# Optimization experiments

Measured on AMD Instinct MI355X. Metric: run time of the kernel, lower is better.

The kernel has to match this reference:

```python
import jax, jax.numpy as jnp
import numpy as np

TOP_K = 2


def setup_inputs() -> dict:
    key = jax.random.key(0)
    k1, k2, k3, k4, k5 = jax.random.split(key, 5)
    B, S, H, F, E = 4, 2048, 1024, 4096, 8
    scale = 1.0 / np.sqrt(H)
    return {
        "hidden_states": jax.random.normal(k1, (B, S, H), dtype=jnp.float32),
        "gate_w": jax.random.normal(k2, (E, H), dtype=jnp.float32) * scale,
        "w1": jax.random.normal(k3, (E, F, H), dtype=jnp.float32) * scale,
        "w3": jax.random.normal(k4, (E, F, H), dtype=jnp.float32) * scale,
        "w2": jax.random.normal(k5, (E, H, F), dtype=jnp.float32) * (1.0 / np.sqrt(F)),
    }


def reference(hidden_states, gate_w, w1, w3, w2):
    B, S, H = hidden_states.shape
    E = gate_w.shape[0]
    x = hidden_states.reshape(-1, H)                    # [T, H], T = B*S

    router_logits = x @ gate_w.T                        # [T, E]
    probs = jax.nn.softmax(router_logits.astype(jnp.float32), axis=-1)
    top_w, top_i = jax.lax.top_k(probs, TOP_K)          # [T, k]
    top_w = top_w / jnp.sum(top_w, axis=-1, keepdims=True)
    top_w = top_w.astype(x.dtype)

    # combine weight of each expert for each token: [E, T]
    one_hot = jax.nn.one_hot(top_i, E, dtype=x.dtype)   # [T, k, E]
    comb = jnp.einsum("tke,tk->et", one_hot, top_w)

    # loop over experts via scan; tokens not routed to expert e have comb==0,
    # which matches the gather/FFN/scatter-combine of the original exactly.
    def body(acc, wts):
        w1e, w3e, w2e, ce = wts
        h = jax.nn.silu(x @ w1e.T) * (x @ w3e.T)        # [T, F]
        return acc + (h @ w2e.T) * ce[:, None], None

    out0 = jnp.zeros_like(x)
    out, _ = jax.lax.scan(body, out0, (w1, w3, w2, comb))
    return out.reshape(B, S, H), router_logits
```

## Files before the change

kernel.cpp:

```cpp
#include <hip/hip_runtime.h>
#include <hip/hip_bf16.h>

#define T_TOK 8192
#define HDIM  1024
#define FDIM  4096
#define NEXP  8
#define CVT_BLKS 2048

typedef __attribute__((ext_vector_type(8))) short short8;
typedef __attribute__((ext_vector_type(4))) float f32x4;
typedef unsigned short u16;
typedef unsigned int   u32;

#define XB_OFF    0ull
#define W1B_OFF   (XB_OFF   + 16777216ull)
#define W3B_OFF   (W1B_OFF  + 67108864ull)
#define W2B_OFF   (W3B_OFF  + 67108864ull)
#define HBUF_OFF  (W2B_OFF  + 67108864ull)
#define CNT_OFF   (HBUF_OFF + 134217728ull)
#define HOFF_OFF  (CNT_OFF  + 64ull)
#define TLIST_OFF (HOFF_OFF + 64ull)
#define WLIST_OFF (TLIST_OFF + 262144ull)
#define WS_NEED   (WLIST_OFF + 262144ull)

__device__ __forceinline__ u16 f2bf(float f) {
  u32 u = __float_as_uint(f);
  return (u16)((u + 0x7fffu + ((u >> 16) & 1u)) >> 16);
}

__device__ __forceinline__ void gl_lds16(const void* g, void* l) {
  __builtin_amdgcn_global_load_lds(
      (const __attribute__((address_space(1))) void*)g,
      (__attribute__((address_space(3))) void*)l, 16, 0, 0);
}

__global__ __launch_bounds__(256) void prep_kernel(
    const float* __restrict__ x, const float* __restrict__ gw,
    const float* __restrict__ s0, const float* __restrict__ s1,
    u16* __restrict__ d0, u16* __restrict__ d1,
    float* __restrict__ logits, u16* __restrict__ xb,
    int* __restrict__ counts, int* __restrict__ tlist, float* __restrict__ wlist) {
  if (blockIdx.x < 8192) {
    const int n8 = NEXP * FDIM * HDIM / 8;
    const int total = 2 * n8;
    const int stride = 8192 * 256;
    for (int i = blockIdx.x * 256 + threadIdx.x; i < total; i += stride) {
      int seg = i >> 22;
      int j = i & (n8 - 1);
      const float* s = seg == 0 ? s0 : s1;
      u16* d = seg == 0 ? d0 : d1;
      float4 v0 = ((const float4*)s)[j * 2];
      float4 v1 = ((const float4*)s)[j * 2 + 1];
      uint4 o;
      o.x = (u32)f2bf(v0.x) | ((u32)f2bf(v0.y) << 16);
      o.y = (u32)f2bf(v0.z) | ((u32)f2bf(v0.w) << 16);
      o.z = (u32)f2bf(v1.x) | ((u32)f2bf(v1.y) << 16);
      o.w = (u32)f2bf(v1.z) | ((u32)f2bf(v1.w) << 16);
      ((uint4*)d)[j] = o;
    }
    return;
  }
  const int wid = threadIdx.x >> 6, lane = threadIdx.x & 63;
  const int t = (blockIdx.x - 8192) * 4 + wid;
  const float* xr = x + (size_t)t * HDIM + lane * 16;
  float4 xv[4];
#pragma unroll
  for (int q = 0; q < 4; ++q) xv[q] = ((const float4*)xr)[q];

  u32 pk[8];
#pragma unroll
  for (int q = 0; q < 4; ++q) {
    pk[q * 2 + 0] = (u32)f2bf(xv[q].x) | ((u32)f2bf(xv[q].y) << 16);
    pk[q * 2 + 1] = (u32)f2bf(xv[q].z) | ((u32)f2bf(xv[q].w) << 16);
  }
  u32* xbo = (u32*)(xb + (size_t)t * HDIM + lane * 16);
  ((uint4*)xbo)[0] = make_uint4(pk[0], pk[1], pk[2], pk[3]);
  ((uint4*)xbo)[1] = make_uint4(pk[4], pk[5], pk[6], pk[7]);

  float lg[NEXP];
#pragma unroll
  for (int e = 0; e < NEXP; ++e) {
    const float4* g = (const float4*)(gw + (size_t)e * HDIM + lane * 16);
    float s = 0.f;
#pragma unroll
    for (int q = 0; q < 4; ++q) {
      float4 gv = g[q];
      s += xv[q].x * gv.x + xv[q].y * gv.y + xv[q].z * gv.z + xv[q].w * gv.w;
    }
#pragma unroll
    for (int off = 32; off > 0; off >>= 1) s += __shfl_xor(s, off, 64);
    lg[e] = s;
  }
  if (lane == 0) {
    float* lo = logits + (size_t)t * NEXP;
#pragma unroll
    for (int e = 0; e < NEXP; ++e) lo[e] = lg[e];
    float v1 = -1e30f, v2 = -1e30f; int i1 = 0, i2 = 0;
#pragma unroll
    for (int e = 0; e < NEXP; ++e) {
      float le = lg[e];
      if (le > v1)      { v2 = v1; i2 = i1; v1 = le; i1 = e; }
      else if (le > v2) { v2 = le; i2 = e; }
    }
    float t2 = __expf(v2 - v1);
    float rs = 1.f / (1.f + t2);
    int p1 = atomicAdd(&counts[i1], 1);
    tlist[i1 * T_TOK + p1] = t; wlist[i1 * T_TOK + p1] = rs;
    int p2 = atomicAdd(&counts[i2], 1);
    tlist[i2 * T_TOK + p2] = t; wlist[i2 * T_TOK + p2] = t2 * rs;
  }
}

__global__ void prefix_kernel(const int* __restrict__ counts, int* __restrict__ hoff) {
  if (threadIdx.x == 0) {
    int s = 0;
    for (int e = 0; e < NEXP; ++e) { hoff[e] = s; s += counts[e]; }
    hoff[NEXP] = s;
  }
}

__global__ __launch_bounds__(256, 4) void ffn1_kernel(
    const u16* __restrict__ xb, const u16* __restrict__ w1b, const u16* __restrict__ w3b,
    u16* __restrict__ hbuf, const int* __restrict__ counts, const int* __restrict__ hoff,
    const int* __restrict__ tlist,
    const float* __restrict__ w2src, u16* __restrict__ w2b) {
  if (blockIdx.x < CVT_BLKS) {
    const int n8 = NEXP * HDIM * FDIM / 8;
    const int stride = CVT_BLKS * 256;
    for (int j = blockIdx.x * 256 + threadIdx.x; j < n8; j += stride) {
      float4 v0 = ((const float4*)w2src)[j * 2];
      float4 v1 = ((const float4*)w2src)[j * 2 + 1];
      uint4 o;
      o.x = (u32)f2bf(v0.x) | ((u32)f2bf(v0.y) << 16);
      o.y = (u32)f2bf(v0.z) | ((u32)f2bf(v0.w) << 16);
      o.z = (u32)f2bf(v1.x) | ((u32)f2bf(v1.y) << 16);
      o.w = (u32)f2bf(v1.z) | ((u32)f2bf(v1.w) << 16);
      ((uint4*)w2b)[j] = o;
    }
    return;
  }
  const int bid = blockIdx.x - CVT_BLKS;
  const int e  = bid & 7;
  const int j  = bid >> 3;
  const int ct = j >> 6;
  const int rt = j & 63;
  const int Ne = counts[e];
  if (rt * 128 >= Ne) return;

  __shared__ u16 LDS[16384];

  const int tid = threadIdx.x;
  const int wid = tid >> 6, lane = tid & 63;
  const int wr = wid >> 1, wc = wid & 1;
  const int lr = lane & 15, lhi = lane >> 4;

  size_t aoff[4];
#pragma unroll
  for (int q = 0; q < 4; ++q) {
    int idx = q * 256 + tid;
    int r = idx >> 3, c = idx & 7;
    int grow = rt * 128 + r;
    int gi = grow < Ne ? grow : Ne - 1;
    aoff[q] = (size_t)tlist[e * T_TOK + gi] * HDIM + (size_t)((c ^ (r & 7)) * 8);
  }
  size_t boff[2];
#pragma unroll
  for (int q = 0; q < 2; ++q) {
    int idx = q * 256 + tid;
    int r = idx >> 3, c = idx & 7;
    boff[q] = ((size_t)e * FDIM + ct * 64 + r) * HDIM + (size_t)((c ^ (r & 7)) * 8);
  }
  const int dW = wid * 64 * 8;

  f32x4 acc1[4][2] = {}, acc3[4][2] = {};

  for (int k0 = 0; k0 < HDIM; k0 += 64) {
    __syncthreads();
#pragma unroll
    for (int q = 0; q < 4; ++q)
      gl_lds16(xb + aoff[q] + k0, LDS + q * 2048 + dW);
#pragma unroll
    for (int q = 0; q < 2; ++q) {
      gl_lds16(w1b + boff[q] + k0, LDS + 8192 + q * 2048 + dW);
      gl_lds16(w3b + boff[q] + k0, LDS + 12288 + q * 2048 + dW);
    }
    __syncthreads();
#pragma unroll
    for (int kk = 0; kk < 2; ++kk) {
      const int chn = ((kk * 4 + lhi) ^ (lr & 7)) * 8;
      short8 af[4], b1f[2], b3f[2];
#pragma unroll
      for (int m = 0; m < 4; ++m)
        af[m] = *(const short8*)(LDS + (wr * 64 + m * 16 + lr) * 64 + chn);
#pragma unroll
      for (int n = 0; n < 2; ++n) {
        int ro = (wc * 32 + n * 16 + lr) * 64 + chn;
        b1f[n] = *(const short8*)(LDS + 8192 + ro);
        b3f[n] = *(const short8*)(LDS + 12288 + ro);
      }
#pragma unroll
      for (int m = 0; m < 4; ++m)
#pragma unroll
        for (int n = 0; n < 2; ++n) {
          acc1[m][n] = __builtin_amdgcn_mfma_f32_16x16x32_bf16(af[m], b1f[n], acc1[m][n], 0, 0, 0);
          acc3[m][n] = __builtin_amdgcn_mfma_f32_16x16x32_bf16(af[m], b3f[n], acc3[m][n], 0, 0, 0);
        }
    }
  }

  const int hb = hoff[e];
  const int rbase = rt * 128 + wr * 64 + lhi * 4;
  const int cbase = ct * 64 + wc * 32 + lr;
#pragma unroll
  for (int m = 0; m < 4; ++m)
#pragma unroll
    for (int i = 0; i < 4; ++i) {
      int grow = rbase + m * 16 + i;
      if (grow < Ne) {
        size_t rowp = (size_t)(hb + grow) * FDIM + cbase;
#pragma unroll
        for (int n = 0; n < 2; ++n) {
          float a1 = acc1[m][n][i], a3 = acc3[m][n][i];
          hbuf[rowp + n * 16] = f2bf((a1 / (1.f + __expf(-a1))) * a3);
        }
      }
    }
}

__global__ __launch_bounds__(256, 4) void ffn2_kernel(
    const u16* __restrict__ hbuf, const u16* __restrict__ w2b,
    float* __restrict__ out, const int* __restrict__ counts, const int* __restrict__ hoff,
    const int* __restrict__ tlist, const float* __restrict__ wlist) {
  const int bid = blockIdx.x;
  const int e  = bid & 7;
  const int j  = bid >> 3;
  const int ct = j >> 6;
  const int rt = j & 63;
  const int Ne = counts[e];
  if (rt * 128 >= Ne) return;
  const int hb = hoff[e];

  __shared__ u16 LDS[12288];

  const int tid = threadIdx.x;
  const int wid = tid >> 6, lane = tid & 63;
  const int wr = wid >> 1, wc = wid & 1;
  const int lr = lane & 15, lhi = lane >> 4;

  size_t aoff[4];
#pragma unroll
  for (int q = 0; q < 4; ++q) {
    int idx = q * 256 + tid;
    int r = idx >> 3, c = idx & 7;
    int grow = rt * 128 + r;
    int gi = grow < Ne ? grow : Ne - 1;
    aoff[q] = (size_t)(hb + gi) * FDIM + (size_t)((c ^ (r & 7)) * 8);
  }
  size_t boff[2];
#pragma unroll
  for (int q = 0; q < 2; ++q) {
    int idx = q * 256 + tid;
    int r = idx >> 3, c = idx & 7;
    boff[q] = ((size_t)e * HDIM + ct * 64 + r) * FDIM + (size_t)((c ^ (r & 7)) * 8);
  }
  const int dW = wid * 64 * 8;

  f32x4 acc[4][2] = {};

  for (int k0 = 0; k0 < FDIM; k0 += 64) {
    __syncthreads();
#pragma unroll
    for (int q = 0; q < 4; ++q)
      gl_lds16(hbuf + aoff[q] + k0, LDS + q * 2048 + dW);
#pragma unroll
    for (int q = 0; q < 2; ++q)
      gl_lds16(w2b + boff[q] + k0, LDS + 8192 + q * 2048 + dW);
    __syncthreads();
#pragma unroll
    for (int kk = 0; kk < 2; ++kk) {
      const int chn = ((kk * 4 + lhi) ^ (lr & 7)) * 8;
      short8 af[4], bf_[2];
#pragma unroll
      for (int m = 0; m < 4; ++m)
        af[m] = *(const short8*)(LDS + (wr * 64 + m * 16 + lr) * 64 + chn);
#pragma unroll
      for (int n = 0; n < 2; ++n)
        bf_[n] = *(const short8*)(LDS + 8192 + (wc * 32 + n * 16 + lr) * 64 + chn);
#pragma unroll
      for (int m = 0; m < 4; ++m)
#pragma unroll
        for (int n = 0; n < 2; ++n)
          acc[m][n] = __builtin_amdgcn_mfma_f32_16x16x32_bf16(af[m], bf_[n], acc[m][n], 0, 0, 0);
    }
  }

  const int rb = rt * 128 + wr * 64 + lhi * 4;
  const int cb = ct * 64 + wc * 32 + lr;
#pragma unroll
  for (int m = 0; m < 4; ++m)
#pragma unroll
    for (int i = 0; i < 4; ++i) {
      int grow = rb + m * 16 + i;
      if (grow < Ne) {
        int tok = tlist[e * T_TOK + grow];
        float wt = wlist[e * T_TOK + grow];
        float* op = out + (size_t)tok * HDIM + cb;
#pragma unroll
        for (int n = 0; n < 2; ++n)
          atomicAdd(op + n * 16, wt * acc[m][n][i]);
      }
    }
}

extern "C" void kernel_launch(void* const* d_in, const int* in_sizes, int n_in,
                              void* d_out, int out_size, void* d_ws, size_t ws_size,
                              hipStream_t stream) {
  (void)in_sizes; (void)n_in; (void)out_size;
  if (ws_size < WS_NEED) return;

  const float* x  = (const float*)d_in[0];
  const float* gw = (const float*)d_in[1];
  const float* w1 = (const float*)d_in[2];
  const float* w3 = (const float*)d_in[3];
  const float* w2 = (const float*)d_in[4];
  float* out = (float*)d_out;
  float* logits = out + (size_t)T_TOK * HDIM;

  char* ws = (char*)d_ws;
  u16* xb    = (u16*)(ws + XB_OFF);
  u16* w1b   = (u16*)(ws + W1B_OFF);
  u16* w3b   = (u16*)(ws + W3B_OFF);
  u16* w2b   = (u16*)(ws + W2B_OFF);
  u16* hbuf  = (u16*)(ws + HBUF_OFF);
  int* counts = (int*)(ws + CNT_OFF);
  int* hoffp  = (int*)(ws + HOFF_OFF);
  int* tlist  = (int*)(ws + TLIST_OFF);
  float* wlist = (float*)(ws + WLIST_OFF);

  hipMemsetAsync(d_out, 0, (size_t)T_TOK * HDIM * sizeof(float), stream);
  hipMemsetAsync(counts, 0, NEXP * sizeof(int), stream);

  prep_kernel<<<8192 + 2048, 256, 0, stream>>>(x, gw, w1, w3, w1b, w3b,
                                               logits, xb, counts, tlist, wlist);
  prefix_kernel<<<1, 64, 0, stream>>>(counts, hoffp);
  ffn1_kernel<<<CVT_BLKS + NEXP * 64 * 64, 256, 0, stream>>>(
      xb, w1b, w3b, hbuf, counts, hoffp, tlist, w2, w2b);
  ffn2_kernel<<<NEXP * 64 * 16, 256, 0, stream>>>(hbuf, w2b, out, counts, hoffp, tlist, wlist);
}
```

Measured before the change: 832.7 us.

## Enlarge FFN GEMM tiles to 256 rows with 512-thread blocks

```diff
diff --git a/kernel.cpp b/kernel.cpp
--- a/kernel.cpp
+++ b/kernel.cpp
@@ -5,7 +5,7 @@
 #define HDIM  1024
 #define FDIM  4096
 #define NEXP  8
-#define CVT_BLKS 2048
+#define CVT_BLKS 1024
 
 typedef __attribute__((ext_vector_type(8))) short short8;
 typedef __attribute__((ext_vector_type(4))) float f32x4;
@@ -119,15 +119,15 @@
   }
 }
 
-__global__ __launch_bounds__(256, 4) void ffn1_kernel(
+__global__ __launch_bounds__(512, 4) void ffn1_kernel(
     const u16* __restrict__ xb, const u16* __restrict__ w1b, const u16* __restrict__ w3b,
     u16* __restrict__ hbuf, const int* __restrict__ counts, const int* __restrict__ hoff,
     const int* __restrict__ tlist,
     const float* __restrict__ w2src, u16* __restrict__ w2b) {
   if (blockIdx.x < CVT_BLKS) {
     const int n8 = NEXP * HDIM * FDIM / 8;
-    const int stride = CVT_BLKS * 256;
-    for (int j = blockIdx.x * 256 + threadIdx.x; j < n8; j += stride) {
+    const int stride = CVT_BLKS * 512;
+    for (int j = blockIdx.x * 512 + threadIdx.x; j < n8; j += stride) {
       float4 v0 = ((const float4*)w2src)[j * 2];
       float4 v1 = ((const float4*)w2src)[j * 2 + 1];
       uint4 o;
@@ -142,165 +142,151 @@
   const int bid = blockIdx.x - CVT_BLKS;
   const int e  = bid & 7;
   const int j  = bid >> 3;
-  const int ct = j >> 6;
-  const int rt = j & 63;
+  const int ct = j >> 5;
+  const int rt = j & 31;
   const int Ne = counts[e];
-  if (rt * 128 >= Ne) return;
-
-  __shared__ u16 LDS[16384];
+  if (rt * 256 >= Ne) return;
+
+  __shared__ u16 LDS[24576];
 
   const int tid = threadIdx.x;
   const int wid = tid >> 6, lane = tid & 63;
-  const int wr = wid >> 1, wc = wid & 1;
+  const int wr = wid >> 2, wc = wid & 3;
   const int lr = lane & 15, lhi = lane >> 4;
 
   size_t aoff[4];
 #pragma unroll
   for (int q = 0; q < 4; ++q) {
-    int idx = q * 256 + tid;
-    int r = idx >> 3, c = idx & 7;
-    int grow = rt * 128 + r;
+    int idx = q * 512 + tid;
+    int s = idx >> 3, c = idx & 7;
+    int grow = rt * 256 + s;
     int gi = grow < Ne ? grow : Ne - 1;
-    aoff[q] = (size_t)tlist[e * T_TOK + gi] * HDIM + (size_t)((c ^ (r & 7)) * 8);
-  }
-  size_t boff[2];
-#pragma unroll
-  for (int q = 0; q < 2; ++q) {
-    int idx = q * 256 + tid;
-    int r = idx >> 3, c = idx & 7;
-    boff[q] = ((size_t)e * FDIM + ct * 64 + r) * HDIM + (size_t)((c ^ (r & 7)) * 8);
-  }
-  const int dW = wid * 64 * 8;
-
-  f32x4 acc1[4][2] = {}, acc3[4][2] = {};
+    aoff[q] = (size_t)tlist[e * T_TOK + gi] * HDIM + (size_t)((c ^ (s & 7)) * 8);
+  }
+  size_t b1off, b3off;
+  {
+    int r = tid >> 3, c = tid & 7;
+    b1off = ((size_t)e * FDIM + ct * 64 + r) * HDIM + (size_t)((c ^ (r & 7)) * 8);
+    b3off = b1off;
+  }
+  const int dW = wid * 512;
+
+  f32x4 acc1[8] = {}, acc3[8] = {};
 
   for (int k0 = 0; k0 < HDIM; k0 += 64) {
     __syncthreads();
 #pragma unroll
     for (int q = 0; q < 4; ++q)
-      gl_lds16(xb + aoff[q] + k0, LDS + q * 2048 + dW);
-#pragma unroll
-    for (int q = 0; q < 2; ++q) {
-      gl_lds16(w1b + boff[q] + k0, LDS + 8192 + q * 2048 + dW);
-      gl_lds16(w3b + boff[q] + k0, LDS + 12288 + q * 2048 + dW);
-    }
+      gl_lds16(xb + aoff[q] + k0, LDS + q * 4096 + dW);
+    gl_lds16(w1b + b1off + k0, LDS + 16384 + dW);
+    gl_lds16(w3b + b3off + k0, LDS + 20480 + dW);
     __syncthreads();
 #pragma unroll
     for (int kk = 0; kk < 2; ++kk) {
       const int chn = ((kk * 4 + lhi) ^ (lr & 7)) * 8;
-      short8 af[4], b1f[2], b3f[2];
-#pragma unroll
-      for (int m = 0; m < 4; ++m)
-        af[m] = *(const short8*)(LDS + (wr * 64 + m * 16 + lr) * 64 + chn);
-#pragma unroll
-      for (int n = 0; n < 2; ++n) {
-        int ro = (wc * 32 + n * 16 + lr) * 64 + chn;
-        b1f[n] = *(const short8*)(LDS + 8192 + ro);
-        b3f[n] = *(const short8*)(LDS + 12288 + ro);
+      short8 af[8], b1v, b3v;
+#pragma unroll
+      for (int m = 0; m < 8; ++m)
+        af[m] = *(const short8*)(LDS + (wr * 128 + m * 16 + lr) * 64 + chn);
+      b1v = *(const short8*)(LDS + 16384 + (wc * 16 + lr) * 64 + chn);
+      b3v = *(const short8*)(LDS + 20480 + (wc * 16 + lr) * 64 + chn);
+#pragma unroll
+      for (int m = 0; m < 8; ++m) {
+        acc1[m] = __builtin_amdgcn_mfma_f32_16x16x32_bf16(af[m], b1v, acc1[m], 0, 0, 0);
+        acc3[m] = __builtin_amdgcn_mfma_f32_16x16x32_bf16(af[m], b3v, acc3[m], 0, 0, 0);
       }
-#pragma unroll
-      for (int m = 0; m < 4; ++m)
-#pragma unroll
-        for (int n = 0; n < 2; ++n) {
-          acc1[m][n] = __builtin_amdgcn_mfma_f32_16x16x32_bf16(af[m], b1f[n], acc1[m][n], 0, 0, 0);
-          acc3[m][n] = __builtin_amdgcn_mfma_f32_16x16x32_bf16(af[m], b3f[n], acc3[m][n], 0, 0, 0);
-        }
     }
   }
 
   const int hb = hoff[e];
-  const int rbase = rt * 128 + wr * 64 + lhi * 4;
-  const int cbase = ct * 64 + wc * 32 + lr;
-#pragma unroll
-  for (int m = 0; m < 4; ++m)
+  const int rbase = rt * 256 + wr * 128 + lhi * 4;
+  const int cb = ct * 64 + wc * 16 + lr;
+#pragma unroll
+  for (int m = 0; m < 8; ++m)
 #pragma unroll
     for (int i = 0; i < 4; ++i) {
       int grow = rbase + m * 16 + i;
       if (grow < Ne) {
-        size_t rowp = (size_t)(hb + grow) * FDIM + cbase;
-#pragma unroll
-        for (int n = 0; n < 2; ++n) {
-          float a1 = acc1[m][n][i], a3 = acc3[m][n][i];
-          hbuf[rowp + n * 16] = f2bf((a1 / (1.f + __expf(-a1))) * a3);
-        }
+        float a1 = acc1[m][i], a3 = acc3[m][i];
+        hbuf[(size_t)(hb + grow) * FDIM + cb] = f2bf((a1 / (1.f + __expf(-a1))) * a3);
       }
     }
 }
 
-__global__ __launch_bounds__(256, 4) void ffn2_kernel(
+__global__ __launch_bounds__(512, 4) void ffn2_kernel(
     const u16* __restrict__ hbuf, const u16* __restrict__ w2b,
     float* __restrict__ out, const int* __restrict__ counts, const int* __restrict__ hoff,
     const int* __restrict__ tlist, const float* __restrict__ wlist) {
   const int bid = blockIdx.x;
   const int e  = bid & 7;
   const int j  = bid >> 3;
-  const int ct = j >> 6;
-  const int rt = j & 63;
+  const int rt = j >> 3;
+  const int ct = j & 7;
   const int Ne = counts[e];
-  if (rt * 128 >= Ne) return;
+  if (rt * 256 >= Ne) return;
   const int hb = hoff[e];
 
-  __shared__ u16 LDS[12288];
+  __shared__ u16 LDS[24576];
 
   const int tid = threadIdx.x;
   const int wid = tid >> 6, lane = tid & 63;
-  const int wr = wid >> 1, wc = wid & 1;
+  const int wr = wid >> 2, wc = wid & 3;
   const int lr = lane & 15, lhi = lane >> 4;
 
   size_t aoff[4];
 #pragma unroll
   for (int q = 0; q < 4; ++q) {
-    int idx = q * 256 + tid;
+    int idx = q * 512 + tid;
+    int s = idx >> 3, c = idx & 7;
+    int grow = rt * 256 + s;
+    int gi = grow < Ne ? grow : Ne - 1;
+    aoff[q] = (size_t)(hb + gi) * FDIM + (size_t)((c ^ (s & 7)) * 8);
+  }
+  size_t boff[2];
+#pragma unroll
+  for (int q = 0; q < 2; ++q) {
+    int idx = q * 512 + tid;
     int r = idx >> 3, c = idx & 7;
-    int grow = rt * 128 + r;
-    int gi = grow < Ne ? grow : Ne - 1;
-    aoff[q] = (size_t)(hb + gi) * FDIM + (size_t)((c ^ (r & 7)) * 8);
-  }
-  size_t boff[2];
-#pragma unroll
-  for (int q = 0; q < 2; ++q) {
-    int idx = q * 256 + tid;
-    int r = idx >> 3, c = idx & 7;
-    boff[q] = ((size_t)e * HDIM + ct * 64 + r) * FDIM + (size_t)((c ^ (r & 7)) * 8);
-  }
-  const int dW = wid * 64 * 8;
-
-  f32x4 acc[4][2] = {};
+    boff[q] = ((size_t)e * HDIM + ct * 128 + r) * FDIM + (size_t)((c ^ (r & 7)) * 8);
+  }
+  const int dW = wid * 512;
+
+  f32x4 acc[8][2] = {};
 
   for (int k0 = 0; k0 < FDIM; k0 += 64) {
     __syncthreads();
 #pragma unroll
     for (int q = 0; q < 4; ++q)
-      gl_lds16(hbuf + aoff[q] + k0, LDS + q * 2048 + dW);
+      gl_lds16(hbuf + aoff[q] + k0, LDS + q * 4096 + dW);
 #pragma unroll
     for (int q = 0; q < 2; ++q)
-      gl_lds16(w2b + boff[q] + k0, LDS + 8192 + q * 2048 + dW);
+      gl_lds16(w2b + boff[q] + k0, LDS + 16384 + q * 4096 + dW);
     __syncthreads();
 #pragma unroll
     for (int kk = 0; kk < 2; ++kk) {
       const int chn = ((kk * 4 + lhi) ^ (lr & 7)) * 8;
-      short8 af[4], bf_[2];
-#pragma unroll
-      for (int m = 0; m < 4; ++m)
-        af[m] = *(const short8*)(LDS + (wr * 64 + m * 16 + lr) * 64 + chn);
+      short8 af[8], bf_[2];
+#pragma unroll
+      for (int m = 0; m < 8; ++m)
+        af[m] = *(const short8*)(LDS + (wr * 128 + m * 16 + lr) * 64 + chn);
 #pragma unroll
       for (int n = 0; n < 2; ++n)
-        bf_[n] = *(const short8*)(LDS + 8192 + (wc * 32 + n * 16 + lr) * 64 + chn);
-#pragma unroll
-      for (int m = 0; m < 4; ++m)
+        bf_[n] = *(const short8*)(LDS + 16384 + (wc * 32 + n * 16 + lr) * 64 + chn);
+#pragma unroll
+      for (int m = 0; m < 8; ++m)
 #pragma unroll
         for (int n = 0; n < 2; ++n)
           acc[m][n] = __builtin_amdgcn_mfma_f32_16x16x32_bf16(af[m], bf_[n], acc[m][n], 0, 0, 0);
     }
   }
 
-  const int rb = rt * 128 + wr * 64 + lhi * 4;
-  const int cb = ct * 64 + wc * 32 + lr;
-#pragma unroll
-  for (int m = 0; m < 4; ++m)
+  const int rbase = rt * 256 + wr * 128 + lhi * 4;
+  const int cb = ct * 128 + wc * 32 + lr;
+#pragma unroll
+  for (int m = 0; m < 8; ++m)
 #pragma unroll
     for (int i = 0; i < 4; ++i) {
-      int grow = rb + m * 16 + i;
+      int grow = rbase + m * 16 + i;
       if (grow < Ne) {
         int tok = tlist[e * T_TOK + grow];
         float wt = wlist[e * T_TOK + grow];
@@ -343,7 +329,7 @@
   prep_kernel<<<8192 + 2048, 256, 0, stream>>>(x, gw, w1, w3, w1b, w3b,
                                                logits, xb, counts, tlist, wlist);
   prefix_kernel<<<1, 64, 0, stream>>>(counts, hoffp);
-  ffn1_kernel<<<CVT_BLKS + NEXP * 64 * 64, 256, 0, stream>>>(
+  ffn1_kernel<<<CVT_BLKS + NEXP * 32 * 64, 512, 0, stream>>>(
       xb, w1b, w3b, hbuf, counts, hoffp, tlist, w2, w2b);
-  ffn2_kernel<<<NEXP * 64 * 16, 256, 0, stream>>>(hbuf, w2b, out, counts, hoffp, tlist, wlist);
-}
+  ffn2_kernel<<<NEXP * 32 * 8, 512, 0, stream>>>(hbuf, w2b, out, counts, hoffp, tlist, wlist);
+}
```

Measured after the change: 929.5 us. +11.6%, slower.

## Replace atomic scatter in FFN2 with bf16 expert output buffer and combine kernel

Applied to the files above, without the earlier changes.

```diff
diff --git a/kernel.cpp b/kernel.cpp
--- a/kernel.cpp
+++ b/kernel.cpp
@@ -27,6 +27,9 @@
   u32 u = __float_as_uint(f);
   return (u16)((u + 0x7fffu + ((u >> 16) & 1u)) >> 16);
 }
+__device__ __forceinline__ float bf2f(u16 v) {
+  return __uint_as_float((u32)v << 16);
+}
 
 __device__ __forceinline__ void gl_lds16(const void* g, void* l) {
   __builtin_amdgcn_global_load_lds(
@@ -39,7 +42,9 @@
     const float* __restrict__ s0, const float* __restrict__ s1,
     u16* __restrict__ d0, u16* __restrict__ d1,
     float* __restrict__ logits, u16* __restrict__ xb,
-    int* __restrict__ counts, int* __restrict__ tlist, float* __restrict__ wlist) {
+    int* __restrict__ counts, int* __restrict__ tlist,
+    float* __restrict__ wt1, float* __restrict__ wt2,
+    int* __restrict__ slot1, int* __restrict__ slot2) {
   if (blockIdx.x < 8192) {
     const int n8 = NEXP * FDIM * HDIM / 8;
     const int total = 2 * n8;
@@ -105,9 +110,11 @@
     float t2 = __expf(v2 - v1);
     float rs = 1.f / (1.f + t2);
     int p1 = atomicAdd(&counts[i1], 1);
-    tlist[i1 * T_TOK + p1] = t; wlist[i1 * T_TOK + p1] = rs;
+    tlist[i1 * T_TOK + p1] = t;
+    slot1[t] = (i1 << 16) | p1;  wt1[t] = rs;
     int p2 = atomicAdd(&counts[i2], 1);
-    tlist[i2 * T_TOK + p2] = t; wlist[i2 * T_TOK + p2] = t2 * rs;
+    tlist[i2 * T_TOK + p2] = t;
+    slot2[t] = (i2 << 16) | p2;  wt2[t] = t2 * rs;
   }
 }
 
@@ -229,8 +236,7 @@
 
 __global__ __launch_bounds__(256, 4) void ffn2_kernel(
     const u16* __restrict__ hbuf, const u16* __restrict__ w2b,
-    float* __restrict__ out, const int* __restrict__ counts, const int* __restrict__ hoff,
-    const int* __restrict__ tlist, const float* __restrict__ wlist) {
+    u16* __restrict__ ybuf, const int* __restrict__ counts, const int* __restrict__ hoff) {
   const int bid = blockIdx.x;
   const int e  = bid & 7;
   const int j  = bid >> 3;
@@ -240,76 +246,88 @@
   if (rt * 128 >= Ne) return;
   const int hb = hoff[e];
 
-  __shared__ u16 LDS[12288];
+  __shared__ u16 Alds[128 * 64];
+  __shared__ u16 Blds[128 * 64];
 
   const int tid = threadIdx.x;
   const int wid = tid >> 6, lane = tid & 63;
   const int wr = wid >> 1, wc = wid & 1;
   const int lr = lane & 15, lhi = lane >> 4;
 
-  size_t aoff[4];
+  size_t aoff[4], boff[4]; int ldso[4];
 #pragma unroll
   for (int q = 0; q < 4; ++q) {
-    int idx = q * 256 + tid;
-    int r = idx >> 3, c = idx & 7;
+    int i = wid * 4 + q;
+    int r = i * 8 + (lane >> 3);
+    int sw = ((lane & 7) ^ (r & 7)) * 8;
     int grow = rt * 128 + r;
     int gi = grow < Ne ? grow : Ne - 1;
-    aoff[q] = (size_t)(hb + gi) * FDIM + (size_t)((c ^ (r & 7)) * 8);
-  }
-  size_t boff[2];
-#pragma unroll
-  for (int q = 0; q < 2; ++q) {
-    int idx = q * 256 + tid;
-    int r = idx >> 3, c = idx & 7;
-    boff[q] = ((size_t)e * HDIM + ct * 64 + r) * FDIM + (size_t)((c ^ (r & 7)) * 8);
-  }
-  const int dW = wid * 64 * 8;
-
-  f32x4 acc[4][2] = {};
+    aoff[q] = (size_t)(hb + gi) * FDIM + sw;
+    int hr = ct * 128 + r;
+    boff[q] = ((size_t)e * HDIM + hr) * FDIM + sw;
+    ldso[q] = i * 512;
+  }
+
+  f32x4 acc[4][4] = {};
 
   for (int k0 = 0; k0 < FDIM; k0 += 64) {
     __syncthreads();
 #pragma unroll
-    for (int q = 0; q < 4; ++q)
-      gl_lds16(hbuf + aoff[q] + k0, LDS + q * 2048 + dW);
-#pragma unroll
-    for (int q = 0; q < 2; ++q)
-      gl_lds16(w2b + boff[q] + k0, LDS + 8192 + q * 2048 + dW);
+    for (int q = 0; q < 4; ++q) {
+      gl_lds16(hbuf + aoff[q] + k0, Alds + ldso[q]);
+      gl_lds16(w2b + boff[q] + k0, Blds + ldso[q]);
+    }
     __syncthreads();
 #pragma unroll
     for (int kk = 0; kk < 2; ++kk) {
-      const int chn = ((kk * 4 + lhi) ^ (lr & 7)) * 8;
-      short8 af[4], bf_[2];
+      const int swo = ((kk * 4 + lhi) ^ (lr & 7)) * 8;
+      short8 af[4], bf_[4];
 #pragma unroll
       for (int m = 0; m < 4; ++m)
-        af[m] = *(const short8*)(LDS + (wr * 64 + m * 16 + lr) * 64 + chn);
-#pragma unroll
-      for (int n = 0; n < 2; ++n)
-        bf_[n] = *(const short8*)(LDS + 8192 + (wc * 32 + n * 16 + lr) * 64 + chn);
+        af[m] = *(const short8*)(Alds + (wr * 64 + m * 16 + lr) * 64 + swo);
+#pragma unroll
+      for (int n = 0; n < 4; ++n)
+        bf_[n] = *(const short8*)(Blds + (wc * 64 + n * 16 + lr) * 64 + swo);
 #pragma unroll
       for (int m = 0; m < 4; ++m)
 #pragma unroll
-        for (int n = 0; n < 2; ++n)
+        for (int n = 0; n < 4; ++n)
           acc[m][n] = __builtin_amdgcn_mfma_f32_16x16x32_bf16(af[m], bf_[n], acc[m][n], 0, 0, 0);
     }
   }
 
   const int rb = rt * 128 + wr * 64 + lhi * 4;
-  const int cb = ct * 64 + wc * 32 + lr;
+  const int cb = ct * 128 + wc * 64 + lr;
 #pragma unroll
   for (int m = 0; m < 4; ++m)
 #pragma unroll
     for (int i = 0; i < 4; ++i) {
       int grow = rb + m * 16 + i;
       if (grow < Ne) {
-        int tok = tlist[e * T_TOK + grow];
-        float wt = wlist[e * T_TOK + grow];
-        float* op = out + (size_t)tok * HDIM + cb;
-#pragma unroll
-        for (int n = 0; n < 2; ++n)
-          atomicAdd(op + n * 16, wt * acc[m][n][i]);
+        u16* yp = ybuf + (size_t)(hb + grow) * HDIM + cb;
+#pragma unroll
+        for (int n = 0; n < 4; ++n)
+          yp[n * 16] = f2bf(acc[m][n][i]);
       }
     }
+}
+
+__global__ __launch_bounds__(256) void combine_kernel(
+    const u16* __restrict__ ybuf, const int* __restrict__ slot1, const int* __restrict__ slot2,
+    const float* __restrict__ wt1, const float* __restrict__ wt2,
+    const int* __restrict__ hoff, float* __restrict__ out) {
+  int idx = blockIdx.x * 256 + threadIdx.x;
+  int t = idx >> 7, c8 = (idx & 127) * 8;
+  int s1 = slot1[t], s2 = slot2[t];
+  float w1 = wt1[t], w2 = wt2[t];
+  size_t r1 = (size_t)(hoff[s1 >> 16] + (s1 & 0xFFFF)) * HDIM + c8;
+  size_t r2 = (size_t)(hoff[s2 >> 16] + (s2 & 0xFFFF)) * HDIM + c8;
+  short8 y1 = *(const short8*)(ybuf + r1);
+  short8 y2 = *(const short8*)(ybuf + r2);
+  float* op = out + (size_t)t * HDIM + c8;
+#pragma unroll
+  for (int k = 0; k < 8; ++k)
+    op[k] = w1 * bf2f((u16)y1[k]) + w2 * bf2f((u16)y2[k]);
 }
 
 extern "C" void kernel_launch(void* const* d_in, const int* in_sizes, int n_in,
@@ -332,18 +350,23 @@
   u16* w3b   = (u16*)(ws + W3B_OFF);
   u16* w2b   = (u16*)(ws + W2B_OFF);
   u16* hbuf  = (u16*)(ws + HBUF_OFF);
+  u16* ybuf  = (u16*)(ws + W1B_OFF);
   int* counts = (int*)(ws + CNT_OFF);
   int* hoffp  = (int*)(ws + HOFF_OFF);
   int* tlist  = (int*)(ws + TLIST_OFF);
-  float* wlist = (float*)(ws + WLIST_OFF);
-
-  hipMemsetAsync(d_out, 0, (size_t)T_TOK * HDIM * sizeof(float), stream);
+  float* wt1  = (float*)(ws + WLIST_OFF);
+  float* wt2  = wt1 + T_TOK;
+  int* slot1  = (int*)(wt2 + T_TOK);
+  int* slot2  = slot1 + T_TOK;
+
   hipMemsetAsync(counts, 0, NEXP * sizeof(int), stream);
 
   prep_kernel<<<8192 + 2048, 256, 0, stream>>>(x, gw, w1, w3, w1b, w3b,
-                                               logits, xb, counts, tlist, wlist);
+                                               logits, xb, counts, tlist,
+                                               wt1, wt2, slot1, slot2);
   prefix_kernel<<<1, 64, 0, stream>>>(counts, hoffp);
   ffn1_kernel<<<CVT_BLKS + NEXP * 64 * 64, 256, 0, stream>>>(
       xb, w1b, w3b, hbuf, counts, hoffp, tlist, w2, w2b);
-  ffn2_kernel<<<NEXP * 64 * 16, 256, 0, stream>>>(hbuf, w2b, out, counts, hoffp, tlist, wlist);
-}
+  ffn2_kernel<<<NEXP * 64 * 8, 256, 0, stream>>>(hbuf, w2b, ybuf, counts, hoffp);
+  combine_kernel<<<T_TOK * 128 / 256, 256, 0, stream>>>(ybuf, slot1, slot2, wt1, wt2, hoffp, out);
+}
```

Measured after the change: 780.8 us. 1.07x faster.
